# Optimization experiments

Measured on AMD Instinct MI355X. Metric: run time of the kernel, lower is better.

The kernel has to match this reference:

```python
import jax, jax.numpy as jnp
import numpy as np

N_NODES = 20000
N_EDGES = 320000
EMB = 128


def setup_inputs() -> dict:
    key = jax.random.key(0)
    ks = jax.random.split(key, 8)
    h = jax.random.normal(ks[0], (N_NODES, EMB), dtype=jnp.float32)
    W1 = jax.random.normal(ks[1], (2 * EMB, 4 * EMB), dtype=jnp.float32) / np.sqrt(2 * EMB)
    b1 = jnp.zeros((4 * EMB,), dtype=jnp.float32)
    W2 = jax.random.normal(ks[2], (4 * EMB, 1), dtype=jnp.float32) / np.sqrt(4 * EMB)
    b2 = jnp.zeros((1,), dtype=jnp.float32)
    # logistic-noise uniforms for RelaxedBernoulli rsample, kept away from {0,1}
    u = jax.random.uniform(ks[3], (N_EDGES,), dtype=jnp.float32, minval=1e-6, maxval=1.0 - 1e-6)
    row = jax.random.randint(ks[4], (N_EDGES,), 0, N_NODES, dtype=jnp.int32)
    col = jax.random.randint(ks[5], (N_EDGES,), 0, N_NODES, dtype=jnp.int32)
    edge_mask = -jnp.ones((N_EDGES,), dtype=jnp.int32)  # torch code initializes mask to -1
    return {"h": h, "W1": W1, "b1": b1, "W2": W2, "b2": b2,
            "u": u, "row": row, "col": col, "edge_mask": edge_mask, "hierarchy": 0}


def _segment_softmax(scores, seg, num_segments):
    m = jax.ops.segment_max(scores, seg, num_segments=num_segments)
    e = jnp.exp(scores - m[seg])
    s = jax.ops.segment_sum(e, seg, num_segments=num_segments)
    return e / s[seg]


TEMPERATURE = 1.0
RATIO = 0.5  # threshold for hard bernoulli


def reference(h, W1, b1, W2, b2, u, row, col, edge_mask, hierarchy):
    # edge gather + concat: [E, 2*EMB]
    edge_rep = jnp.concatenate([h[row], h[col]], axis=-1)
    # 2-layer MLP edge scorer -> [E]
    hid = jax.nn.relu(edge_rep @ W1 + b1)
    scores = (hid @ W2 + b2).reshape(-1)
    # segment softmax over edges grouped by source node (torch: softmax(edge_score, edge_index[0]))
    probs = _segment_softmax(scores, row, N_NODES)
    # RelaxedBernoulli(temperature, probs).rsample(): sigmoid((logits + logistic)/T)
    logits = jnp.log(probs) - jnp.log1p(-probs)
    logistic = jnp.log(u) - jnp.log1p(-u)
    y = jax.nn.sigmoid((logits + logistic) / TEMPERATURE)
    y_hard = (y > RATIO).astype(y.dtype)
    y_st = jax.lax.stop_gradient(y_hard - y) + y  # straight-through
    # edge_mask[y == 1] = hierarchy + 1
    new_mask = jnp.where(y_st == 1.0, jnp.int32(hierarchy + 1), edge_mask)
    c_idx = new_mask > 0
    s_idx = new_mask == -1
    causal_w = jnp.where(c_idx, scores, 0.0)
    spu_w = jnp.where(s_idx, -scores, 0.0)
    return scores, y_st, new_mask, causal_w, spu_w
```

## Files before the change

### kernel.cpp

```cpp
#include <hip/hip_runtime.h>
#include <math.h>

#define N_NODES 20000
#define N_EDGES 320000
#define EMB 128
#define HID 512
#define ROWS_PER_BLOCK 16
#define SC_CAP 2048
#define NCHUNK ((N_NODES + 1023) / 1024)

typedef float v2f __attribute__((ext_vector_type(2)));

#if defined(__has_builtin)
#if __has_builtin(__builtin_elementwise_fma)
#define V2FMA(a, b, c) __builtin_elementwise_fma((a), (b), (c))
#else
#define V2FMA(a, b, c) ((a) * (b) + (c))
#endif
#else
#define V2FMA(a, b, c) ((a) * (b) + (c))
#endif

__global__ void init_deg(int* __restrict__ deg, int* __restrict__ offs) {
    int i = blockIdx.x * 256 + threadIdx.x;
    if (i < N_NODES) deg[i] = 0;
    if (i == 0) offs[N_NODES] = N_EDGES;
}

#define TM 128
#define TN 128
#define BK 8
#define NTILES (EMB / BK)
#define GEMM_MT ((N_NODES + TM - 1) / TM)
#define GEMM_BLOCKS (8 * GEMM_MT)
#define HIST_BLOCKS ((N_EDGES + 255) / 256)

__global__ __launch_bounds__(256) void gemm_hist(
    const float* __restrict__ h, const float* __restrict__ W1,
    const float* __restrict__ b1, float* __restrict__ P, float* __restrict__ Q,
    const int* __restrict__ row, int* __restrict__ deg)
{
    const int bid = blockIdx.x;
    const int tid = threadIdx.x;

    if (bid >= GEMM_BLOCKS) {
        const int e = (bid - GEMM_BLOCKS) * 256 + tid;
        if (e < N_EDGES) atomicAdd(&deg[row[e]], 1);
        return;
    }

    __shared__ float As[2][BK][TM + 4];
    __shared__ float Bs[2][BK][TN];

    const int nt = bid & 7;
    const int mt = bid >> 3;
    const int m_base = mt * TM;

    const int a_m = tid >> 1;
    const int a_k = (tid & 1) << 2;
    const int  row_a = m_base + a_m;
    const bool a_ok  = row_a < N_NODES;
    const float* __restrict__ hrow = h + (size_t)row_a * EMB + a_k;

    const int b_k = tid >> 5;
    const int b_n = (tid & 31) << 2;
    const int w_row_off = (nt < 4) ? 0 : 128;
    const int w_col     = (nt & 3) * TN + b_n;
    const float* __restrict__ wrow = W1 + (size_t)(w_row_off + b_k) * HID + w_col;

    const int ty = tid >> 4, tx = tid & 15;
    const int cm = ty << 2, cn = tx << 2;

    v2f acc[8][4] = {};

    float4 pa, pb;
    pa = make_float4(0.f, 0.f, 0.f, 0.f);
    if (a_ok) pa = *(const float4*)(hrow);
    pb = *(const float4*)(wrow);
    As[0][a_k + 0][a_m] = pa.x;
    As[0][a_k + 1][a_m] = pa.y;
    As[0][a_k + 2][a_m] = pa.z;
    As[0][a_k + 3][a_m] = pa.w;
    *(float4*)&Bs[0][b_k][b_n] = pb;
    __syncthreads();

    for (int t = 0; t < NTILES; ++t) {
        const int cur = t & 1;
        if (t + 1 < NTILES) {
            const int k0 = (t + 1) * BK;
            pa = make_float4(0.f, 0.f, 0.f, 0.f);
            if (a_ok) pa = *(const float4*)(hrow + k0);
            pb = *(const float4*)(wrow + (size_t)k0 * HID);
        }

#pragma unroll
        for (int kk = 0; kk < BK; ++kk) {
            float a[8];
            *(float4*)&a[0] = *(const float4*)&As[cur][kk][cm];
            *(float4*)&a[4] = *(const float4*)&As[cur][kk][cm + 64];
            float4 b0 = *(const float4*)&Bs[cur][kk][cn];
            float4 b1v = *(const float4*)&Bs[cur][kk][cn + 64];
            v2f bp[4] = {(v2f){b0.x, b0.y}, (v2f){b0.z, b0.w},
                         (v2f){b1v.x, b1v.y}, (v2f){b1v.z, b1v.w}};
#pragma unroll
            for (int i = 0; i < 8; ++i) {
                v2f ai = (v2f){a[i], a[i]};
#pragma unroll
                for (int j = 0; j < 4; ++j)
                    acc[i][j] = V2FMA(ai, bp[j], acc[i][j]);
            }
        }

        if (t + 1 < NTILES) {
            const int nxt = 1 - cur;
            As[nxt][a_k + 0][a_m] = pa.x;
            As[nxt][a_k + 1][a_m] = pa.y;
            As[nxt][a_k + 2][a_m] = pa.z;
            As[nxt][a_k + 3][a_m] = pa.w;
            *(float4*)&Bs[nxt][b_k][b_n] = pb;
            __syncthreads();
        }
    }

    const bool  isP = (nt < 4);
    const int   col_base = (nt & 3) * TN;
    float* __restrict__ dstbase = isP ? P : Q;

    v2f bias[4] = {{0.f,0.f},{0.f,0.f},{0.f,0.f},{0.f,0.f}};
    if (isP) {
        float4 bv0 = *(const float4*)(b1 + col_base + cn);
        float4 bv1 = *(const float4*)(b1 + col_base + cn + 64);
        bias[0] = (v2f){bv0.x, bv0.y};
        bias[1] = (v2f){bv0.z, bv0.w};
        bias[2] = (v2f){bv1.x, bv1.y};
        bias[3] = (v2f){bv1.z, bv1.w};
    }

#pragma unroll
    for (int i = 0; i < 8; ++i) {
        const int r = m_base + cm + (i < 4 ? i : 64 + i - 4);
        if (r < N_NODES) {
            float* dst = dstbase + (size_t)r * HID + col_base;
            v2f c0 = acc[i][0] + bias[0], c1 = acc[i][1] + bias[1];
            v2f c2 = acc[i][2] + bias[2], c3 = acc[i][3] + bias[3];
            *(float4*)(dst + cn)      = make_float4(c0.x, c0.y, c1.x, c1.y);
            *(float4*)(dst + cn + 64) = make_float4(c2.x, c2.y, c3.x, c3.y);
        }
    }
}

__device__ __forceinline__ int wave_incl_scan(int v, int lane) {
#pragma unroll
    for (int off = 1; off < 64; off <<= 1) {
        int t = __shfl_up(v, off, 64);
        if (lane >= off) v += t;
    }
    return v;
}

__global__ __launch_bounds__(1024) void scan_part(const int* __restrict__ deg,
                                                  int* __restrict__ part,
                                                  int* __restrict__ totals) {
    __shared__ int wsum[16];
    const int tid = threadIdx.x, lane = tid & 63, w = tid >> 6;
    const int i = blockIdx.x * 1024 + tid;
    int v = (i < N_NODES) ? deg[i] : 0;
    int incl = wave_incl_scan(v, lane);
    if (lane == 63) wsum[w] = incl;
    __syncthreads();
    if (w == 0) {
        int x = (lane < 16) ? wsum[lane] : 0;
        int xs = wave_incl_scan(x, lane);
        if (lane < 16) wsum[lane] = xs - x;
        if (lane == 15) totals[blockIdx.x] = xs;
    }
    __syncthreads();
    if (i < N_NODES) part[i] = wsum[w] + incl - v;
}

__global__ __launch_bounds__(1024) void scan_apply(const int* __restrict__ part,
                                                   const int* __restrict__ totals,
                                                   int* __restrict__ cursor,
                                                   int* __restrict__ offs) {
    __shared__ int carry_s;
    const int tid = threadIdx.x;
    if (tid < 64) {
        int v = (tid < NCHUNK) ? totals[tid] : 0;
        int incl = wave_incl_scan(v, tid);
        if (tid == (int)blockIdx.x) carry_s = incl - v;
    }
    __syncthreads();
    const int i = blockIdx.x * 1024 + tid;
    if (i < N_NODES) {
        int o = part[i] + carry_s;
        cursor[i] = o;
        offs[i] = o;
    }
}

__global__ void scatter_edges(const int* __restrict__ row, const int* __restrict__ col,
                              int* __restrict__ cursor, int2* __restrict__ rc2) {
    int e = blockIdx.x * 256 + threadIdx.x;
    if (e >= N_EDGES) return;
    int r = row[e];
    int pos = atomicAdd(&cursor[r], 1);
    rc2[pos] = make_int2(e, (r << 16) | col[e]);
}

__global__ __launch_bounds__(256) void fused_edge(
    const float* __restrict__ P, const float* __restrict__ Q,
    const float* __restrict__ W2, const float* __restrict__ b2,
    const int2* __restrict__ rc2, const int* __restrict__ offs,
    const float* __restrict__ u, const int* __restrict__ edge_mask,
    const int* __restrict__ hierarchy,
    float* __restrict__ scores, float* __restrict__ out_y,
    float* __restrict__ out_mask, float* __restrict__ out_causal,
    float* __restrict__ out_spu)
{
    __shared__ float sc_lds[SC_CAP];

    const int r0 = blockIdx.x * ROWS_PER_BLOCK;
    const int r1 = (r0 + ROWS_PER_BLOCK < N_NODES) ? r0 + ROWS_PER_BLOCK : N_NODES;
    const int e0 = offs[r0];
    const int e1 = offs[r1];
    const int tid = threadIdx.x, lane = tid & 63, w = tid >> 6;
    const int j0 = lane << 2;

    const float4 w0 = *(const float4*)(W2 + j0);
    const float4 w1 = *(const float4*)(W2 + 256 + j0);
    const float bias2 = b2[0];

    for (int i0 = e0 + (w << 1); i0 < e1; i0 += 8) {
        const int  iA   = i0;
        const bool hasB = (i0 + 1) < e1;
        const int  iB   = hasB ? i0 + 1 : i0;

        const int2 eA = rc2[iA];
        const int2 eB = rc2[iB];
        const int rA = ((unsigned)eA.y) >> 16, cA = eA.y & 0xFFFF;
        const int rB = ((unsigned)eB.y) >> 16, cB = eB.y & 0xFFFF;
        const float* __restrict__ pA = P + (size_t)rA * HID;
        const float* __restrict__ qA = Q + (size_t)cA * HID;
        const float* __restrict__ pB = P + (size_t)rB * HID;
        const float* __restrict__ qB = Q + (size_t)cB * HID;

        float4 pA0 = *(const float4*)(pA + j0);
        float4 pA1 = *(const float4*)(pA + 256 + j0);
        float4 qA0 = *(const float4*)(qA + j0);
        float4 qA1 = *(const float4*)(qA + 256 + j0);
        float4 pB0 = *(const float4*)(pB + j0);
        float4 pB1 = *(const float4*)(pB + 256 + j0);
        float4 qB0 = *(const float4*)(qB + j0);
        float4 qB1 = *(const float4*)(qB + 256 + j0);

        float sA = 0.0f, sB = 0.0f;
        sA = fmaf(fmaxf(pA0.x + qA0.x, 0.0f), w0.x, sA);
        sA = fmaf(fmaxf(pA0.y + qA0.y, 0.0f), w0.y, sA);
        sA = fmaf(fmaxf(pA0.z + qA0.z, 0.0f), w0.z, sA);
        sA = fmaf(fmaxf(pA0.w + qA0.w, 0.0f), w0.w, sA);
        sA = fmaf(fmaxf(pA1.x + qA1.x, 0.0f), w1.x, sA);
        sA = fmaf(fmaxf(pA1.y + qA1.y, 0.0f), w1.y, sA);
        sA = fmaf(fmaxf(pA1.z + qA1.z, 0.0f), w1.z, sA);
        sA = fmaf(fmaxf(pA1.w + qA1.w, 0.0f), w1.w, sA);
        sB = fmaf(fmaxf(pB0.x + qB0.x, 0.0f), w0.x, sB);
        sB = fmaf(fmaxf(pB0.y + qB0.y, 0.0f), w0.y, sB);
        sB = fmaf(fmaxf(pB0.z + qB0.z, 0.0f), w0.z, sB);
        sB = fmaf(fmaxf(pB0.w + qB0.w, 0.0f), w0.w, sB);
        sB = fmaf(fmaxf(pB1.x + qB1.x, 0.0f), w1.x, sB);
        sB = fmaf(fmaxf(pB1.y + qB1.y, 0.0f), w1.y, sB);
        sB = fmaf(fmaxf(pB1.z + qB1.z, 0.0f), w1.z, sB);
        sB = fmaf(fmaxf(pB1.w + qB1.w, 0.0f), w1.w, sB);

#pragma unroll
        for (int off = 32; off > 0; off >>= 1) {
            sA += __shfl_down(sA, off, 64);
            sB += __shfl_down(sB, off, 64);
        }

        if (lane == 0) {
            float scA = sA + bias2;
            scores[eA.x] = scA;
            int liA = iA - e0;
            if (liA < SC_CAP) sc_lds[liA] = scA;
            if (hasB) {
                float scB = sB + bias2;
                scores[eB.x] = scB;
                int liB = iB - e0;
                if (liB < SC_CAP) sc_lds[liB] = scB;
            }
        }
    }
    __syncthreads();

    const int hv = hierarchy[0];
    for (int r = r0 + w; r < r1; r += 4) {
        const int es = offs[r], ee = offs[r + 1];
        const int d = ee - es;
        if (d == 0) continue;

        float m = -INFINITY;
        for (int j = lane; j < d; j += 64) {
            int li = es - e0 + j;
            float s = (li < SC_CAP) ? sc_lds[li] : scores[rc2[es + j].x];
            m = fmaxf(m, s);
        }
#pragma unroll
        for (int off = 32; off > 0; off >>= 1)
            m = fmaxf(m, __shfl_down(m, off, 64));
        m = __shfl(m, 0, 64);

        float ssum = 0.0f;
        for (int j = lane; j < d; j += 64) {
            int li = es - e0 + j;
            float s = (li < SC_CAP) ? sc_lds[li] : scores[rc2[es + j].x];
            ssum += expf(s - m);
        }
#pragma unroll
        for (int off = 32; off > 0; off >>= 1)
            ssum += __shfl_down(ssum, off, 64);
        ssum = __shfl(ssum, 0, 64);

        for (int j = lane; j < d; j += 64) {
            int li = es - e0 + j;
            float s = (li < SC_CAP) ? sc_lds[li] : scores[rc2[es + j].x];
            float p = expf(s - m) / ssum;
            float logits = logf(p) - log1pf(-p);
            int oe = rc2[es + j].x;
            float uu = u[oe];
            float L = logf(uu) - log1pf(-uu);
            float y = 1.0f / (1.0f + expf(-(logits + L)));
            bool hard = y > 0.5f;
            int mm = hard ? (hv + 1) : edge_mask[oe];
            out_y[oe]      = hard ? 1.0f : 0.0f;
            out_mask[oe]   = (float)mm;
            out_causal[oe] = (mm > 0)   ?  s : 0.0f;
            out_spu[oe]    = (mm == -1) ? -s : 0.0f;
        }
    }
}

extern "C" void kernel_launch(void* const* d_in, const int* in_sizes, int n_in,
                              void* d_out, int out_size, void* d_ws, size_t ws_size,
                              hipStream_t stream) {
    const float* h_ptr = (const float*)d_in[0];
    const float* W1    = (const float*)d_in[1];
    const float* b1    = (const float*)d_in[2];
    const float* W2    = (const float*)d_in[3];
    const float* b2    = (const float*)d_in[4];
    const float* u     = (const float*)d_in[5];
    const int*   row   = (const int*)d_in[6];
    const int*   col   = (const int*)d_in[7];
    const int*   emask = (const int*)d_in[8];
    const int*   hier  = (const int*)d_in[9];

    float* out        = (float*)d_out;
    float* scores     = out;
    float* out_y      = out + (size_t)N_EDGES;
    float* out_mask   = out + 2 * (size_t)N_EDGES;
    float* out_causal = out + 3 * (size_t)N_EDGES;
    float* out_spu    = out + 4 * (size_t)N_EDGES;

    float* P      = (float*)d_ws;
    float* Qm     = P + (size_t)N_NODES * HID;
    int2*  rc2    = (int2*)(Qm + (size_t)N_NODES * HID);
    int*   deg    = (int*)(rc2 + N_EDGES);
    int*   cursor = deg + N_NODES;
    int*   offs   = cursor + N_NODES;
    int*   part   = offs + N_NODES + 1;
    int*   totals = part + N_NODES;

    hipLaunchKernelGGL(init_deg, dim3((N_NODES + 255) / 256), dim3(256), 0, stream,
                       deg, offs);

    hipLaunchKernelGGL(gemm_hist, dim3(GEMM_BLOCKS + HIST_BLOCKS), dim3(256), 0, stream,
                       h_ptr, W1, b1, P, Qm, row, deg);

    hipLaunchKernelGGL(scan_part, dim3(NCHUNK), dim3(1024), 0, stream, deg, part, totals);
    hipLaunchKernelGGL(scan_apply, dim3(NCHUNK), dim3(1024), 0, stream,
                       part, totals, cursor, offs);
    hipLaunchKernelGGL(scatter_edges, dim3((N_EDGES + 255) / 256), dim3(256), 0, stream,
                       row, col, cursor, rc2);

    hipLaunchKernelGGL(fused_edge, dim3((N_NODES + ROWS_PER_BLOCK - 1) / ROWS_PER_BLOCK),
                       dim3(256), 0, stream,
                       P, Qm, W2, b2, rc2, offs, u, emask, hier,
                       scores, out_y, out_mask, out_causal, out_spu);
}
```

Measured before the change: 286.5 us.

## Replace shared-memory tiled GEMM with per-lane row, wave-uniform weight-broadcast GEMM

Replaces the 128x128 shared-memory double-buffered tile GEMM that computes the node projections P and Q with a scheme where each lane owns one node row and each wave owns 64 output columns. Weights are read directly from global memory with wave-uniform addresses, so they can become scalar or broadcast loads, and no LDS or block barriers are needed. The cost is that each thread reads its own h row with strided per-lane float4 loads (uncoalesced across the wave) and holds 64 accumulators. The whole weight matrix is also re-read per block from cache, with less register-tile reuse than the 8x8 outer product.

Result: slower. 542.0 us (+89.2%).

```diff
diff --git a/kernel.cpp b/kernel.cpp
--- a/kernel.cpp
+++ b/kernel.cpp
@@ -27,12 +27,9 @@
     if (i == 0) offs[N_NODES] = N_EDGES;
 }
 
-#define TM 128
-#define TN 128
-#define BK 8
-#define NTILES (EMB / BK)
-#define GEMM_MT ((N_NODES + TM - 1) / TM)
-#define GEMM_BLOCKS (8 * GEMM_MT)
+#define GX 4
+#define GY ((N_NODES + 63) / 64)
+#define GEMM_BLOCKS (GX * GY)
 #define HIST_BLOCKS ((N_EDGES + 255) / 256)
 
 __global__ __launch_bounds__(256) void gemm_hist(
@@ -49,102 +46,54 @@
         return;
     }
 
-    __shared__ float As[2][BK][TM + 4];
-    __shared__ float Bs[2][BK][TN];
-
-    const int nt = bid & 7;
-    const int mt = bid >> 3;
-    const int m_base = mt * TM;
-
-    const int a_m = tid >> 1;
-    const int a_k = (tid & 1) << 2;
-    const int  row_a = m_base + a_m;
-    const bool a_ok  = row_a < N_NODES;
-    const float* __restrict__ hrow = h + (size_t)row_a * EMB + a_k;
-
-    const int b_k = tid >> 5;
-    const int b_n = (tid & 31) << 2;
-    const int w_row_off = (nt < 4) ? 0 : 128;
-    const int w_col     = (nt & 3) * TN + b_n;
-    const float* __restrict__ wrow = W1 + (size_t)(w_row_off + b_k) * HID + w_col;
-
-    const int ty = tid >> 4, tx = tid & 15;
-    const int cm = ty << 2, cn = tx << 2;
-
-    v2f acc[8][4] = {};
-
-    float4 pa, pb;
-    pa = make_float4(0.f, 0.f, 0.f, 0.f);
-    if (a_ok) pa = *(const float4*)(hrow);
-    pb = *(const float4*)(wrow);
-    As[0][a_k + 0][a_m] = pa.x;
-    As[0][a_k + 1][a_m] = pa.y;
-    As[0][a_k + 2][a_m] = pa.z;
-    As[0][a_k + 3][a_m] = pa.w;
-    *(float4*)&Bs[0][b_k][b_n] = pb;
-    __syncthreads();
-
-    for (int t = 0; t < NTILES; ++t) {
-        const int cur = t & 1;
-        if (t + 1 < NTILES) {
-            const int k0 = (t + 1) * BK;
-            pa = make_float4(0.f, 0.f, 0.f, 0.f);
-            if (a_ok) pa = *(const float4*)(hrow + k0);
-            pb = *(const float4*)(wrow + (size_t)k0 * HID);
-        }
-
-#pragma unroll
-        for (int kk = 0; kk < BK; ++kk) {
-            float a[8];
-            *(float4*)&a[0] = *(const float4*)&As[cur][kk][cm];
-            *(float4*)&a[4] = *(const float4*)&As[cur][kk][cm + 64];
-            float4 b0 = *(const float4*)&Bs[cur][kk][cn];
-            float4 b1v = *(const float4*)&Bs[cur][kk][cn + 64];
-            v2f bp[4] = {(v2f){b0.x, b0.y}, (v2f){b0.z, b0.w},
-                         (v2f){b1v.x, b1v.y}, (v2f){b1v.z, b1v.w}};
-#pragma unroll
-            for (int i = 0; i < 8; ++i) {
-                v2f ai = (v2f){a[i], a[i]};
-#pragma unroll
-                for (int j = 0; j < 4; ++j)
-                    acc[i][j] = V2FMA(ai, bp[j], acc[i][j]);
+    const int bx = bid & 3;
+    const int by = bid >> 2;
+    const int w  = tid >> 6;
+    const int lane = tid & 63;
+
+    const int g0  = bx * 256 + w * 64;
+    const bool isP = (g0 < HID);
+    const int w_off = isP ? 0 : EMB;
+    const int c0    = isP ? g0 : g0 - HID;
+    const float* __restrict__ wbase = W1 + (size_t)w_off * HID + c0;
+
+    const int  r   = by * 64 + lane;
+    const bool rok = r < N_NODES;
+    const float* __restrict__ hrow = h + (size_t)(rok ? r : 0) * EMB;
+
+    v2f acc[32] = {};
+
+    float4 a4 = *(const float4*)(hrow);
+    for (int k0 = 0; k0 < EMB; k0 += 4) {
+        float4 a_n = a4;
+        if (k0 + 4 < EMB) a_n = *(const float4*)(hrow + k0 + 4);
+        const float av[4] = {a4.x, a4.y, a4.z, a4.w};
+#pragma unroll
+        for (int kk = 0; kk < 4; ++kk) {
+            const float* __restrict__ wrow = wbase + (size_t)(k0 + kk) * HID;
+            const v2f a2 = (v2f){av[kk], av[kk]};
+#pragma unroll
+            for (int j = 0; j < 32; ++j) {
+                v2f b = *(const v2f*)(wrow + j * 2);
+                acc[j] = V2FMA(a2, b, acc[j]);
             }
         }
-
-        if (t + 1 < NTILES) {
-            const int nxt = 1 - cur;
-            As[nxt][a_k + 0][a_m] = pa.x;
-            As[nxt][a_k + 1][a_m] = pa.y;
-            As[nxt][a_k + 2][a_m] = pa.z;
-            As[nxt][a_k + 3][a_m] = pa.w;
-            *(float4*)&Bs[nxt][b_k][b_n] = pb;
-            __syncthreads();
-        }
-    }
-
-    const bool  isP = (nt < 4);
-    const int   col_base = (nt & 3) * TN;
-    float* __restrict__ dstbase = isP ? P : Q;
-
-    v2f bias[4] = {{0.f,0.f},{0.f,0.f},{0.f,0.f},{0.f,0.f}};
-    if (isP) {
-        float4 bv0 = *(const float4*)(b1 + col_base + cn);
-        float4 bv1 = *(const float4*)(b1 + col_base + cn + 64);
-        bias[0] = (v2f){bv0.x, bv0.y};
-        bias[1] = (v2f){bv0.z, bv0.w};
-        bias[2] = (v2f){bv1.x, bv1.y};
-        bias[3] = (v2f){bv1.z, bv1.w};
-    }
-
-#pragma unroll
-    for (int i = 0; i < 8; ++i) {
-        const int r = m_base + cm + (i < 4 ? i : 64 + i - 4);
-        if (r < N_NODES) {
-            float* dst = dstbase + (size_t)r * HID + col_base;
-            v2f c0 = acc[i][0] + bias[0], c1 = acc[i][1] + bias[1];
-            v2f c2 = acc[i][2] + bias[2], c3 = acc[i][3] + bias[3];
-            *(float4*)(dst + cn)      = make_float4(c0.x, c0.y, c1.x, c1.y);
-            *(float4*)(dst + cn + 64) = make_float4(c2.x, c2.y, c3.x, c3.y);
+        a4 = a_n;
+    }
+
+    if (rok) {
+        if (isP) {
+#pragma unroll
+            for (int j = 0; j < 32; ++j) {
+                v2f b = *(const v2f*)(b1 + c0 + j * 2);
+                acc[j] += b;
+            }
+        }
+        float* __restrict__ dst = (isP ? P : Q) + (size_t)r * HID + c0;
+#pragma unroll
+        for (int j = 0; j < 16; ++j) {
+            *(float4*)(dst + j * 4) =
+                make_float4(acc[2*j].x, acc[2*j].y, acc[2*j+1].x, acc[2*j+1].y);
         }
     }
 }
```
